# Performance work log

Hardware: AMD Instinct MI355X
Metric: run time of the kernel (lower is better)

The kernel has to match this reference:

```python
import jax, jax.numpy as jnp
import numpy as np

N = 50000
E = 800000
DIM = 256
HEADS = 4
HDIM = DIM // HEADS  # 64
NEG_SLOPE = 0.2
LN_EPS = 1e-5


def _layernorm(x, g, b):
    mu = jnp.mean(x, axis=-1, keepdims=True)
    var = jnp.var(x, axis=-1, keepdims=True)
    return (x - mu) * jax.lax.rsqrt(var + LN_EPS) * g + b


def setup_inputs() -> dict:
    key = jax.random.key(0)
    ks = jax.random.split(key, 10)
    x = jax.random.normal(ks[0], (N, DIM), dtype=jnp.float32)
    edge_index = jax.random.randint(ks[1], (2, E), 0, N, dtype=jnp.int64)
    s = 0.05
    W = jax.random.normal(ks[2], (DIM, DIM), dtype=jnp.float32) * s       # GAT linear (heads*out = dim)
    a_src = jax.random.normal(ks[3], (HEADS, HDIM), dtype=jnp.float32) * s
    a_dst = jax.random.normal(ks[4], (HEADS, HDIM), dtype=jnp.float32) * s
    gat_b = jnp.zeros((DIM,), dtype=jnp.float32)
    ln_g = jnp.ones((DIM,), dtype=jnp.float32)
    ln_b = jnp.zeros((DIM,), dtype=jnp.float32)
    W1 = jax.random.normal(ks[5], (DIM, 4 * DIM), dtype=jnp.float32) * s
    b1 = jnp.zeros((4 * DIM,), dtype=jnp.float32)
    W2 = jax.random.normal(ks[6], (4 * DIM, DIM), dtype=jnp.float32) * s
    b2 = jnp.zeros((DIM,), dtype=jnp.float32)
    return {"x": x, "edge_index": edge_index, "W": W, "a_src": a_src,
            "a_dst": a_dst, "gat_b": gat_b, "ln_g": ln_g, "ln_b": ln_b,
            "W1": W1, "b1": b1, "W2": W2, "b2": b2}


def _gat(x, edge_index, W, a_src, a_dst, gat_b):
    # project and split heads: [N, H, C]
    h = (x @ W).reshape(N, HEADS, HDIM)
    alpha_src = jnp.einsum('nhc,hc->nh', h, a_src)  # [N, H]
    alpha_dst = jnp.einsum('nhc,hc->nh', h, a_dst)  # [N, H]
    src = edge_index[0]
    dst = edge_index[1]
    e = jax.nn.leaky_relu(alpha_src[src] + alpha_dst[dst], NEG_SLOPE)  # [E, H]
    # segment softmax over edges sharing a destination node
    m = jax.ops.segment_max(e, dst, num_segments=N)                   # [N, H]
    ex = jnp.exp(e - m[dst])
    denom = jax.ops.segment_sum(ex, dst, num_segments=N)              # [N, H]
    alpha = ex / (denom[dst] + 1e-16)                                 # [E, H]
    msg = h[src] * alpha[:, :, None]                                  # [E, H, C]
    out = jax.ops.segment_sum(msg.reshape(E, DIM), dst, num_segments=N)
    return out + gat_b


def reference(x, edge_index, W, a_src, a_dst, gat_b, ln_g, ln_b, W1, b1, W2, b2):
    residual = x
    g = _gat(x, edge_index, W, a_src, a_dst, gat_b)
    x = _layernorm(x + g, ln_g, ln_b)
    ffn = jax.nn.gelu(x @ W1 + b1, approximate=False) @ W2 + b2
    x = _layernorm(x + ffn, ln_g, ln_b)  # same norm params reused, as in source
    return x + residual
```

## Files before the change

kernel.cpp:

```cpp
#include <hip/hip_runtime.h>
#include <hip/hip_bf16.h>
#include <math.h>

typedef __bf16 bf16;
typedef bf16 bf16x8 __attribute__((ext_vector_type(8)));
typedef float floatx4 __attribute__((ext_vector_type(4)));

#define NN 50000
#define EE 800000
#define DIMC 256
#define FFC 1024

typedef __attribute__((address_space(3))) unsigned int lds_u32;
typedef __attribute__((address_space(1))) unsigned int gbl_u32;

static __device__ __forceinline__ void glds16(const bf16* g, bf16* l) {
    __builtin_amdgcn_global_load_lds((const gbl_u32*)g, (lds_u32*)l, 16, 0, 0);
}

static __device__ __forceinline__ unsigned short f2b(float f) {
    bf16 b = (bf16)f;
    return __builtin_bit_cast(unsigned short, b);
}
static __device__ __forceinline__ float b2f_lo(unsigned u) { return __uint_as_float(u << 16); }
static __device__ __forceinline__ float b2f_hi(unsigned u) { return __uint_as_float(u & 0xffff0000u); }

static __device__ __forceinline__ float gelu_f(float v) {
    float z = -1.5957691216f * v - 0.0713548163f * v * v * v;
    return v / (1.f + __expf(z));
}

__global__ __launch_bounds__(256)
void k_cast_bf16(const float* __restrict__ in, bf16* __restrict__ out, long n4) {
    long i = (long)blockIdx.x * 256 + threadIdx.x;
    if (i >= n4) return;
    float4 v = ((const float4*)in)[i];
    uint2 p;
    p.x = (unsigned)f2b(v.x) | ((unsigned)f2b(v.y) << 16);
    p.y = (unsigned)f2b(v.z) | ((unsigned)f2b(v.w) << 16);
    ((uint2*)out)[i] = p;
}

__global__ __launch_bounds__(256)
void k_tcast(const float* __restrict__ in, bf16* __restrict__ out, int K, int Nc) {
    __shared__ float t[32][33];
    int n0 = blockIdx.x * 32, k0 = blockIdx.y * 32;
    int tx = threadIdx.x & 31, ty = threadIdx.x >> 5;
#pragma unroll
    for (int i = 0; i < 4; ++i)
        t[ty + i * 8][tx] = in[(long)(k0 + ty + i * 8) * Nc + n0 + tx];
    __syncthreads();
#pragma unroll
    for (int i = 0; i < 4; ++i)
        out[(long)(n0 + ty + i * 8) * K + k0 + tx] = (bf16)t[tx][ty + i * 8];
}

template <int EPI>
__global__ __launch_bounds__(256)
void k_gemmA(const bf16* __restrict__ A, const bf16* __restrict__ BT,
             bf16* __restrict__ C, const float* __restrict__ bias,
             const float* __restrict__ avs, const float* __restrict__ avd,
             float* __restrict__ asrcO, float* __restrict__ adstO,
             int M, int K, int Nc) {
    __shared__ __attribute__((aligned(16))) bf16 smem[17408];
    bf16* As = smem;
    bf16* Bs = smem + 8192;
    const int tid = threadIdx.x;
    const int w = tid >> 6, lane = tid & 63;
    const int gm = blockIdx.x * 128, gn = blockIdx.y * 128;
    const int wm = (w >> 1) * 64, wn = (w & 1) * 64;
    const int lr = lane & 15, lkc = lane >> 4;

    long aoff[4], boff[4];
#pragma unroll
    for (int j = 0; j < 4; ++j) {
        int s = w * 4 + j;
        int r = s * 8 + (lane >> 3);
        int kc = ((lane & 7) ^ (r & 7)) * 8;
        aoff[j] = (long)min(gm + r, M - 1) * K + kc;
        boff[j] = (long)(gn + r) * K + kc;
    }

    floatx4 acc[4][4];
#pragma unroll
    for (int a = 0; a < 4; ++a)
#pragma unroll
        for (int b = 0; b < 4; ++b) acc[a][b] = floatx4{0.f, 0.f, 0.f, 0.f};

    for (int k0 = 0; k0 < K; k0 += 64) {
        if (k0) __syncthreads();
#pragma unroll
        for (int j = 0; j < 4; ++j) {
            int s = w * 4 + j;
            glds16(A + aoff[j] + k0, As + s * 512);
            glds16(BT + boff[j] + k0, Bs + s * 512);
        }
        __syncthreads();
#pragma unroll
        for (int kk = 0; kk < 2; ++kk) {
            bf16x8 af[4], bv[4];
#pragma unroll
            for (int mi = 0; mi < 4; ++mi) {
                int r = wm + mi * 16 + lr;
                int ch = (kk * 4 + lkc) ^ (r & 7);
                af[mi] = *(const bf16x8*)(As + r * 64 + ch * 8);
            }
#pragma unroll
            for (int ni = 0; ni < 4; ++ni) {
                int r = wn + ni * 16 + lr;
                int ch = (kk * 4 + lkc) ^ (r & 7);
                bv[ni] = *(const bf16x8*)(Bs + r * 64 + ch * 8);
            }
#pragma unroll
            for (int mi = 0; mi < 4; ++mi)
#pragma unroll
                for (int ni = 0; ni < 4; ++ni)
                    acc[mi][ni] = __builtin_amdgcn_mfma_f32_16x16x32_bf16(af[mi], bv[ni], acc[mi][ni], 0, 0, 0);
        }
    }

    __syncthreads();
    bf16* cs = smem;
#pragma unroll
    for (int ni = 0; ni < 4; ++ni) {
        const int cl = wn + ni * 16 + lr;
        const float bvs = (EPI == 1) ? bias[gn + cl] : 0.f;
#pragma unroll
        for (int mi = 0; mi < 4; ++mi)
#pragma unroll
            for (int i = 0; i < 4; ++i) {
                int rl = wm + mi * 16 + lkc * 4 + i;
                float v = acc[mi][ni][i] + bvs;
                if (EPI == 1) v = gelu_f(v);
                cs[rl * 136 + cl] = (bf16)v;
            }
    }
    __syncthreads();

    const int c8 = (lane & 15) * 8;
    float as8[8], ad8[8];
    int hd = 0;
    if (EPI == 0) {
        hd = (gn >> 6) + ((lane & 15) >> 3);
        const int cb = hd * 64 + (c8 & 63);
#pragma unroll
        for (int i = 0; i < 8; ++i) { as8[i] = avs[cb + i]; ad8[i] = avd[cb + i]; }
    }

#pragma unroll
    for (int t = 0; t < 8; ++t) {
        int rl = w * 32 + t * 4 + (lane >> 4);
        int grow = gm + rl;
        uint4 val = *(const uint4*)(cs + rl * 136 + c8);
        if (grow < M) *(uint4*)(C + (long)grow * Nc + gn + c8) = val;
        if (EPI == 0) {
            float h0 = b2f_lo(val.x), h1 = b2f_hi(val.x), h2 = b2f_lo(val.y), h3 = b2f_hi(val.y);
            float h4 = b2f_lo(val.z), h5 = b2f_hi(val.z), h6 = b2f_lo(val.w), h7 = b2f_hi(val.w);
            float ds = h0 * as8[0] + h1 * as8[1] + h2 * as8[2] + h3 * as8[3]
                     + h4 * as8[4] + h5 * as8[5] + h6 * as8[6] + h7 * as8[7];
            float dd = h0 * ad8[0] + h1 * ad8[1] + h2 * ad8[2] + h3 * ad8[3]
                     + h4 * ad8[4] + h5 * ad8[5] + h6 * ad8[6] + h7 * ad8[7];
#pragma unroll
            for (int off = 1; off < 8; off <<= 1) { ds += __shfl_xor(ds, off); dd += __shfl_xor(dd, off); }
            if ((lane & 7) == 0 && grow < M) {
                asrcO[grow * 4 + hd] = ds;
                adstO[grow * 4 + hd] = dd;
            }
        }
    }
}

__global__ __launch_bounds__(512)
void k_ffn(const bf16* __restrict__ x1b, const bf16* __restrict__ W1T,
           const bf16* __restrict__ W2T, const float* __restrict__ b1,
           const float* __restrict__ b2, const float* __restrict__ x,
           const float* __restrict__ lng, const float* __restrict__ lnb,
           float* __restrict__ out, int M) {
    __shared__ __attribute__((aligned(16))) bf16 smem[18432];
    bf16* acts = smem;
    bf16* w1s  = smem + 2048;
    bf16* w2s  = smem + 10240;
    const int tid = threadIdx.x;
    const int w = tid >> 6, lane = tid & 63;
    const int lr = lane & 15, lkc = lane >> 4;
    const int mg = w >> 1, nh = w & 1;
    const int gm = blockIdx.x * 64;

    bf16x8 xf[8];
    {
        long rb = (long)min(gm + mg * 16 + lr, M - 1) * DIMC;
#pragma unroll
        for (int kf = 0; kf < 8; ++kf)
            xf[kf] = *(const bf16x8*)(x1b + rb + kf * 32 + lkc * 8);
    }

    floatx4 accB[8];
#pragma unroll
    for (int i = 0; i < 8; ++i) accB[i] = floatx4{0.f, 0.f, 0.f, 0.f};

    for (int c = 0; c < 32; ++c) {
        if (c) __syncthreads();
#pragma unroll
        for (int j = 0; j < 2; ++j) {
            int sg = w * 2 + j;
            int r = sg * 2 + (lane >> 5);
            int col = ((lane & 31) ^ (r & 7)) * 8;
            glds16(W1T + (long)(c * 32 + r) * DIMC + col, w1s + sg * 512);
        }
#pragma unroll
        for (int j = 0; j < 2; ++j) {
            int sg = w * 2 + j;
            int r = sg * 16 + (lane >> 2);
            int col = c * 32 + (((lane & 3) ^ ((r >> 1) & 3)) * 8);
            glds16(W2T + (long)r * FFC + col, w2s + sg * 512);
        }
        __syncthreads();

        floatx4 accA = floatx4{0.f, 0.f, 0.f, 0.f};
        const int rbA = nh * 16 + lr;
#pragma unroll
        for (int kf = 0; kf < 8; ++kf) {
            int g = (kf * 4 + lkc) ^ (rbA & 7);
            bf16x8 bv = *(const bf16x8*)(w1s + rbA * 256 + g * 8);
            accA = __builtin_amdgcn_mfma_f32_16x16x32_bf16(xf[kf], bv, accA, 0, 0, 0);
        }
        float b1v = b1[c * 32 + nh * 16 + lr];
#pragma unroll
        for (int i = 0; i < 4; ++i) {
            int row = mg * 16 + lkc * 4 + i;
            int colc = nh * 16 + lr;
            int g = (colc >> 3) ^ ((row >> 1) & 3);
            acts[row * 32 + g * 8 + (colc & 7)] = (bf16)gelu_f(accA[i] + b1v);
        }
        __syncthreads();

        {
            int ra = mg * 16 + lr;
            int ga = lkc ^ ((ra >> 1) & 3);
            bf16x8 af = *(const bf16x8*)(acts + ra * 32 + ga * 8);
#pragma unroll
            for (int ni = 0; ni < 8; ++ni) {
                int rb = nh * 128 + ni * 16 + lr;
                int gb = lkc ^ ((rb >> 1) & 3);
                bf16x8 bv = *(const bf16x8*)(w2s + rb * 32 + gb * 8);
                accB[ni] = __builtin_amdgcn_mfma_f32_16x16x32_bf16(af, bv, accB[ni], 0, 0, 0);
            }
        }
    }

    __syncthreads();
    bf16* cs = smem;
#pragma unroll
    for (int ni = 0; ni < 8; ++ni) {
        int col = nh * 128 + ni * 16 + lr;
        float b2v = b2[col];
#pragma unroll
        for (int i = 0; i < 4; ++i) {
            int rl = mg * 16 + lkc * 4 + i;
            cs[rl * 264 + col] = (bf16)(accB[ni][i] + b2v);
        }
    }
    __syncthreads();
    float4 g4 = *(const float4*)(lng + lane * 4);
    float4 lb4 = *(const float4*)(lnb + lane * 4);
#pragma unroll 1
    for (int t = 0; t < 8; ++t) {
        int r = w * 8 + t;
        int grow = gm + r;
        long base = (long)min(grow, M - 1) * DIMC + lane * 4;
        uint2 cu = *(const uint2*)(cs + r * 264 + lane * 4);
        uint2 xu = *(const uint2*)(x1b + base);
        float v0 = b2f_lo(cu.x) + b2f_lo(xu.x);
        float v1 = b2f_hi(cu.x) + b2f_hi(xu.x);
        float v2 = b2f_lo(cu.y) + b2f_lo(xu.y);
        float v3 = b2f_hi(cu.y) + b2f_hi(xu.y);
        float s1 = v0 + v1 + v2 + v3;
        float s2 = v0 * v0 + v1 * v1 + v2 * v2 + v3 * v3;
#pragma unroll
        for (int off = 1; off < 64; off <<= 1) { s1 += __shfl_xor(s1, off); s2 += __shfl_xor(s2, off); }
        float mu = s1 * (1.f / DIMC);
        float rs = rsqrtf(s2 * (1.f / DIMC) - mu * mu + 1e-5f);
        float4 xr = *(const float4*)(x + base);
        float4 o;
        o.x = (v0 - mu) * rs * g4.x + lb4.x + xr.x;
        o.y = (v1 - mu) * rs * g4.y + lb4.y + xr.y;
        o.z = (v2 - mu) * rs * g4.z + lb4.z + xr.z;
        o.w = (v3 - mu) * rs * g4.w + lb4.w + xr.w;
        if (grow < M) *(float4*)(out + (long)grow * DIMC + lane * 4) = o;
    }
}

__global__ __launch_bounds__(256)
void k_count(const int* __restrict__ dst, unsigned* __restrict__ deg) {
    int e = blockIdx.x * 256 + threadIdx.x;
    if (e < EE) atomicAdd(&deg[dst[e]], 1u);
}

__global__ __launch_bounds__(1024)
void k_scan(const unsigned* __restrict__ deg, unsigned* __restrict__ rowoff,
            unsigned* __restrict__ cursor) {
    __shared__ unsigned wsum[16], wscan[16];
    __shared__ unsigned carry;
    int tid = threadIdx.x, lane = tid & 63, wid = tid >> 6;
    if (tid == 0) carry = 0;
    __syncthreads();
    for (int base = 0; base < NN; base += 1024) {
        int i = base + tid;
        unsigned v = (i < NN) ? deg[i] : 0u;
        unsigned s = v;
        for (int off = 1; off < 64; off <<= 1) {
            unsigned t = __shfl_up(s, off);
            if (lane >= off) s += t;
        }
        if (lane == 63) wsum[wid] = s;
        __syncthreads();
        if (wid == 0) {
            unsigned t = (lane < 16) ? wsum[lane] : 0u;
            unsigned ts = t;
            for (int off = 1; off < 16; off <<= 1) {
                unsigned u2 = __shfl_up(ts, off);
                if (lane >= off) ts += u2;
            }
            if (lane < 16) wscan[lane] = ts;
        }
        __syncthreads();
        unsigned basew = (wid > 0) ? wscan[wid - 1] : 0u;
        unsigned excl = carry + basew + (s - v);
        if (i < NN) { rowoff[i] = excl; cursor[i] = excl; }
        __syncthreads();
        if (tid == 0) carry += wscan[15];
        __syncthreads();
    }
    if (tid == 0) rowoff[NN] = carry;
}

__global__ __launch_bounds__(256)
void k_fill(const int* __restrict__ src, const int* __restrict__ dst,
            unsigned* __restrict__ cursor, unsigned* __restrict__ elist) {
    int e = blockIdx.x * 256 + threadIdx.x;
    if (e < EE) {
        unsigned p = atomicAdd(&cursor[dst[e]], 1u);
        elist[p] = (unsigned)src[e];
    }
}

__global__ __launch_bounds__(256)
void k_agg_ln1(const unsigned* __restrict__ rowoff, const unsigned* __restrict__ elist,
               const float* __restrict__ asrc, const float* __restrict__ adst,
               const bf16* __restrict__ hb, const float* __restrict__ x,
               const float* __restrict__ gatb, const float* __restrict__ lng,
               const float* __restrict__ lnb, bf16* __restrict__ x1b) {
    int node = (blockIdx.x * 256 + threadIdx.x) >> 6;
    int lane = threadIdx.x & 63;
    if (node >= NN) return;
    int beg = (int)rowoff[node], end = (int)rowoff[node + 1];
    int head = lane >> 4;
    float ad = adst[node * 4 + head];
    const int c = lane * 4;
    const bf16* hc = hb + c;
    const int bl = lane & 48;

    float dsum = 0.f;
    float a0 = 0.f, a1 = 0.f, a2 = 0.f, a3 = 0.f;

    for (int c0 = beg; c0 < end; c0 += 16) {
        int take = end - c0; if (take > 16) take = 16;
        int jj = c0 + (lane & 15);
        float ex = 0.f; int s = 0;
        if (jj < end) {
            s = (int)elist[jj];
            float e = asrc[s * 4 + head] + ad;
            e = (e > 0.f) ? e : 0.2f * e;
            ex = __expf(e);
        }
        dsum += ex;
        if (take == 16) {
#pragma unroll
            for (int j = 0; j < 16; ++j) {
                float al = __shfl(ex, bl + j);
                int sj = __shfl(s, bl + j);
                uint2 u = *(const uint2*)(hc + (long)sj * DIMC);
                a0 += al * b2f_lo(u.x);
                a1 += al * b2f_hi(u.x);
                a2 += al * b2f_lo(u.y);
                a3 += al * b2f_hi(u.y);
            }
        } else {
            for (int j = 0; j < take; ++j) {
                float al = __shfl(ex, bl + j);
                int sj = __shfl(s, bl + j);
                uint2 u = *(const uint2*)(hc + (long)sj * DIMC);
                a0 += al * b2f_lo(u.x);
                a1 += al * b2f_hi(u.x);
                a2 += al * b2f_lo(u.y);
                a3 += al * b2f_hi(u.y);
            }
        }
    }
    dsum += __shfl_xor(dsum, 1);
    dsum += __shfl_xor(dsum, 2);
    dsum += __shfl_xor(dsum, 4);
    dsum += __shfl_xor(dsum, 8);
    float invd = 1.f / (dsum + 1e-16f);
    a0 *= invd; a1 *= invd; a2 *= invd; a3 *= invd;

    long base = (long)node * DIMC + c;
    float4 xr = *(const float4*)(x + base);
    float4 gb = *(const float4*)(gatb + c);
    float v0 = xr.x + a0 + gb.x;
    float v1 = xr.y + a1 + gb.y;
    float v2 = xr.z + a2 + gb.z;
    float v3 = xr.w + a3 + gb.w;
    float s1 = v0 + v1 + v2 + v3;
    float s2 = v0 * v0 + v1 * v1 + v2 * v2 + v3 * v3;
    for (int off = 1; off < 64; off <<= 1) { s1 += __shfl_xor(s1, off); s2 += __shfl_xor(s2, off); }
    float mu = s1 * (1.f / DIMC);
    float rs = rsqrtf(s2 * (1.f / DIMC) - mu * mu + 1e-5f);
    float4 g4 = *(const float4*)(lng + c);
    float4 b4 = *(const float4*)(lnb + c);
    float y0 = (v0 - mu) * rs * g4.x + b4.x;
    float y1 = (v1 - mu) * rs * g4.y + b4.y;
    float y2 = (v2 - mu) * rs * g4.z + b4.z;
    float y3 = (v3 - mu) * rs * g4.w + b4.w;
    uint2 p;
    p.x = (unsigned)f2b(y0) | ((unsigned)f2b(y1) << 16);
    p.y = (unsigned)f2b(y2) | ((unsigned)f2b(y3) << 16);
    *(uint2*)(x1b + base) = p;
}

extern "C" void kernel_launch(void* const* d_in, const int* in_sizes, int n_in,
                              void* d_out, int out_size, void* d_ws, size_t ws_size,
                              hipStream_t stream) {
    const float* x    = (const float*)d_in[0];
    const int*   ei   = (const int*)d_in[1];
    const float* W    = (const float*)d_in[2];
    const float* a_s  = (const float*)d_in[3];
    const float* a_d  = (const float*)d_in[4];
    const float* gatb = (const float*)d_in[5];
    const float* lng  = (const float*)d_in[6];
    const float* lnb  = (const float*)d_in[7];
    const float* W1   = (const float*)d_in[8];
    const float* b1   = (const float*)d_in[9];
    const float* W2   = (const float*)d_in[10];
    const float* b2   = (const float*)d_in[11];
    float* out = (float*)d_out;
    char* ws = (char*)d_ws;

    bf16*     xb     = (bf16*)(ws + 0L);
    bf16*     hb     = (bf16*)(ws + 25600000L);
    bf16*     x1b    = (bf16*)(ws + 51200000L);
    float*    asrc   = (float*)(ws + 179200000L);
    float*    adst   = (float*)(ws + 180000000L);
    unsigned* deg    = (unsigned*)(ws + 180800000L);
    unsigned* cursor = (unsigned*)(ws + 181000192L);
    unsigned* rowoff = (unsigned*)(ws + 181200384L);
    unsigned* elist  = (unsigned*)(ws + 181400832L);
    bf16*     WT     = (bf16*)(ws + 184600832L);
    bf16*     W1T    = (bf16*)(ws + 184731904L);
    bf16*     W2T    = (bf16*)(ws + 185256192L);

    const int* esrc = ei;
    const int* edst = ei + EE;

    hipMemsetAsync(deg, 0, NN * sizeof(unsigned), stream);
    k_cast_bf16<<<12500, 256, 0, stream>>>(x, xb, (long)NN * DIMC / 4);
    {
        dim3 gw(DIMC / 32, DIMC / 32);
        k_tcast<<<gw, 256, 0, stream>>>(W, WT, DIMC, DIMC);
        dim3 gw1(FFC / 32, DIMC / 32);
        k_tcast<<<gw1, 256, 0, stream>>>(W1, W1T, DIMC, FFC);
        dim3 gw2(DIMC / 32, FFC / 32);
        k_tcast<<<gw2, 256, 0, stream>>>(W2, W2T, FFC, DIMC);
    }

    dim3 g1(391, 2);
    k_gemmA<0><<<g1, 256, 0, stream>>>(xb, WT, hb, nullptr, a_s, a_d, asrc, adst, NN, DIMC, DIMC);

    k_count<<<3125, 256, 0, stream>>>(edst, deg);
    k_scan<<<1, 1024, 0, stream>>>(deg, rowoff, cursor);
    k_fill<<<3125, 256, 0, stream>>>(esrc, edst, cursor, elist);

    k_agg_ln1<<<12500, 256, 0, stream>>>(rowoff, elist, asrc, adst, hb, x, gatb, lng, lnb, x1b);

    k_ffn<<<782, 512, 0, stream>>>(x1b, W1T, W2T, b1, b2, x, lng, lnb, out, NN);
}
```

Measured before the change: 502.0 us.

## Double-buffer FFN weight tiles in LDS with async prefetch of next chunk

The FFN kernel now stages W1/W2 chunks into two LDS buffers, prefetching chunk c+1 with global_load_lds while chunk c is computed, and uses partial vmcnt waits with raw s_barrier in place of full syncthreads. It also splits the first GEMM into two independent MFMA accumulator chains, stages b1 in LDS, and stores GELU activations as fp32 in a swizzled LDS buffer. The aim is to hide global-load latency behind MFMA work and shorten dependency chains. In exchange LDS use roughly doubles, which can cut occupancy, and the hand-written waitcnt/barrier ordering is fragile.

```diff
diff --git a/kernel.cpp b/kernel.cpp
--- a/kernel.cpp
+++ b/kernel.cpp
@@ -170,16 +170,34 @@
     }
 }
 
+#define STAGE_W(cc, pp) do {                                                    \
+    bf16* w1d = smem + (pp) * 8192;                                             \
+    bf16* w2d = smem + 16384 + (pp) * 8192;                                     \
+    _Pragma("unroll")                                                           \
+    for (int j = 0; j < 2; ++j) {                                               \
+        int sg = w * 2 + j;                                                     \
+        int r = sg * 2 + (lane >> 5);                                           \
+        int col = ((lane & 31) ^ (r & 7)) * 8;                                  \
+        glds16(W1T + (long)((cc) * 32 + r) * DIMC + col, w1d + sg * 512);       \
+    }                                                                           \
+    _Pragma("unroll")                                                           \
+    for (int j = 0; j < 2; ++j) {                                               \
+        int sg = w * 2 + j;                                                     \
+        int r = sg * 16 + (lane >> 2);                                          \
+        int col = (cc) * 32 + (((lane & 3) ^ ((r >> 1) & 3)) * 8);              \
+        glds16(W2T + (long)r * FFC + col, w2d + sg * 512);                      \
+    }                                                                           \
+} while (0)
+
 __global__ __launch_bounds__(512)
 void k_ffn(const bf16* __restrict__ x1b, const bf16* __restrict__ W1T,
            const bf16* __restrict__ W2T, const float* __restrict__ b1,
            const float* __restrict__ b2, const float* __restrict__ x,
            const float* __restrict__ lng, const float* __restrict__ lnb,
            float* __restrict__ out, int M) {
-    __shared__ __attribute__((aligned(16))) bf16 smem[18432];
-    bf16* acts = smem;
-    bf16* w1s  = smem + 2048;
-    bf16* w2s  = smem + 10240;
+    __shared__ __attribute__((aligned(16))) bf16 smem[38912];
+    float* actf = (float*)(smem + 32768);
+    float* b1sf = (float*)(smem + 36864);
     const int tid = threadIdx.x;
     const int w = tid >> 6, lane = tid & 63;
     const int lr = lane & 15, lkc = lane >> 4;
@@ -193,59 +211,68 @@
         for (int kf = 0; kf < 8; ++kf)
             xf[kf] = *(const bf16x8*)(x1b + rb + kf * 32 + lkc * 8);
     }
+    if (w < 4) glds16((const bf16*)(b1 + (long)tid * 4), (bf16*)(b1sf + w * 256));
+    STAGE_W(0, 0);
 
     floatx4 accB[8];
 #pragma unroll
     for (int i = 0; i < 8; ++i) accB[i] = floatx4{0.f, 0.f, 0.f, 0.f};
 
+    const int rbA = nh * 16 + lr;
+    const int rAct = mg * 16 + lr;
+    const int kAct = nh * 16 + lr;
+
+#pragma unroll 2
     for (int c = 0; c < 32; ++c) {
-        if (c) __syncthreads();
-#pragma unroll
-        for (int j = 0; j < 2; ++j) {
-            int sg = w * 2 + j;
-            int r = sg * 2 + (lane >> 5);
-            int col = ((lane & 31) ^ (r & 7)) * 8;
-            glds16(W1T + (long)(c * 32 + r) * DIMC + col, w1s + sg * 512);
-        }
-#pragma unroll
-        for (int j = 0; j < 2; ++j) {
-            int sg = w * 2 + j;
-            int r = sg * 16 + (lane >> 2);
-            int col = c * 32 + (((lane & 3) ^ ((r >> 1) & 3)) * 8);
-            glds16(W2T + (long)r * FFC + col, w2s + sg * 512);
-        }
-        __syncthreads();
-
-        floatx4 accA = floatx4{0.f, 0.f, 0.f, 0.f};
-        const int rbA = nh * 16 + lr;
-#pragma unroll
-        for (int kf = 0; kf < 8; ++kf) {
-            int g = (kf * 4 + lkc) ^ (rbA & 7);
-            bf16x8 bv = *(const bf16x8*)(w1s + rbA * 256 + g * 8);
-            accA = __builtin_amdgcn_mfma_f32_16x16x32_bf16(xf[kf], bv, accA, 0, 0, 0);
-        }
-        float b1v = b1[c * 32 + nh * 16 + lr];
+        const int p = c & 1;
+        const int cn = (c < 31) ? (c + 1) : 31;
+        STAGE_W(cn, (c + 1) & 1);
+        asm volatile("s_waitcnt vmcnt(4)" ::: "memory");
+        __builtin_amdgcn_s_barrier();
+        asm volatile("" ::: "memory");
+
+        bf16* w1p = smem + p * 8192;
+        bf16* w2p = smem + 16384 + p * 8192;
+
+        floatx4 a0 = floatx4{0.f, 0.f, 0.f, 0.f}, a1 = a0;
+#pragma unroll
+        for (int kf = 0; kf < 8; kf += 2) {
+            int g0 = (kf * 4 + lkc) ^ (rbA & 7);
+            int g1 = ((kf + 1) * 4 + lkc) ^ (rbA & 7);
+            bf16x8 bva = *(const bf16x8*)(w1p + rbA * 256 + g0 * 8);
+            bf16x8 bvb = *(const bf16x8*)(w1p + rbA * 256 + g1 * 8);
+            a0 = __builtin_amdgcn_mfma_f32_16x16x32_bf16(xf[kf], bva, a0, 0, 0, 0);
+            a1 = __builtin_amdgcn_mfma_f32_16x16x32_bf16(xf[kf + 1], bvb, a1, 0, 0, 0);
+        }
+        float b1v = b1sf[c * 32 + kAct];
 #pragma unroll
         for (int i = 0; i < 4; ++i) {
-            int row = mg * 16 + lkc * 4 + i;
-            int colc = nh * 16 + lr;
-            int g = (colc >> 3) ^ ((row >> 1) & 3);
-            acts[row * 32 + g * 8 + (colc & 7)] = (bf16)gelu_f(accA[i] + b1v);
-        }
-        __syncthreads();
+            int r = mg * 16 + lkc * 4 + i;
+            float v = gelu_f(a0[i] + a1[i] + b1v);
+            actf[r * 32 + (((kAct >> 2) ^ (r & 7)) << 2) + (kAct & 3)] = v;
+        }
+        asm volatile("s_waitcnt lgkmcnt(0)" ::: "memory");
+        __builtin_amdgcn_s_barrier();
+        asm volatile("" ::: "memory");
 
         {
-            int ra = mg * 16 + lr;
-            int ga = lkc ^ ((ra >> 1) & 3);
-            bf16x8 af = *(const bf16x8*)(acts + ra * 32 + ga * 8);
+            int g0 = (lkc * 2) ^ (rAct & 7);
+            int g1 = (lkc * 2 + 1) ^ (rAct & 7);
+            float4 lo = *(const float4*)(actf + rAct * 32 + g0 * 4);
+            float4 hi = *(const float4*)(actf + rAct * 32 + g1 * 4);
+            bf16x8 af;
+            af[0] = (bf16)lo.x; af[1] = (bf16)lo.y; af[2] = (bf16)lo.z; af[3] = (bf16)lo.w;
+            af[4] = (bf16)hi.x; af[5] = (bf16)hi.y; af[6] = (bf16)hi.z; af[7] = (bf16)hi.w;
 #pragma unroll
             for (int ni = 0; ni < 8; ++ni) {
                 int rb = nh * 128 + ni * 16 + lr;
                 int gb = lkc ^ ((rb >> 1) & 3);
-                bf16x8 bv = *(const bf16x8*)(w2s + rb * 32 + gb * 8);
+                bf16x8 bv = *(const bf16x8*)(w2p + rb * 32 + gb * 8);
                 accB[ni] = __builtin_amdgcn_mfma_f32_16x16x32_bf16(af, bv, accB[ni], 0, 0, 0);
             }
         }
+        __builtin_amdgcn_s_barrier();
+        asm volatile("" ::: "memory");
     }
 
     __syncthreads();
```

Result: slower. 530.3 us (+5.6%).
